# Kernel tuning notes

Hardware: AMD Instinct MI355X
Metric: run time of the kernel (lower is better)

Reference implementation:

```python
import jax, jax.numpy as jnp
import numpy as np


def setup_inputs() -> dict:
    key = jax.random.key(0)
    ks = jax.random.split(key, 8)
    B, L, I, H, O = 512, 512, 256, 1024, 1
    def glorot(k, shape, fan_sum):
        return jax.random.uniform(k, shape, jnp.float32, -1.0, 1.0) * (6.0 / fan_sum) ** 0.5
    return {
        "X": jax.random.normal(ks[0], (B, L, I), jnp.float32),
        "W_in1": glorot(ks[1], (H, I), H + I),
        "b_in1": jnp.zeros((H, 1), jnp.float32),
        "W_rec1": glorot(ks[2], (H, H), H + H),
        "W_in2": glorot(ks[3], (H, I), H + I),
        "b_in2": jnp.zeros((H, 1), jnp.float32),
        "W_rec2": glorot(ks[4], (H, H), H + H),
        "W_out": glorot(ks[5], (O, H), O + H),
        "b_out": jnp.zeros((O, 1), jnp.float32),
    }


def reference(X, W_in1, b_in1, W_rec1, W_in2, b_in2, W_rec2, W_out, b_out):
    B, L, I = X.shape
    H = W_in1.shape[0]
    Xs = jnp.swapaxes(X, 0, 1)  # (L, B, I)
    # Precompute the input-to-hidden projections for all timesteps (parallel GEMMs).
    in1 = jnp.einsum("hi,lbi->lbh", W_in1, Xs) + b_in1[:, 0]  # (L, B, H)
    in2 = jnp.einsum("hi,lbi->lbh", W_in2, Xs) + b_in2[:, 0]  # (L, B, H)
    even = (jnp.arange(L) % 2 == 0)[:, None, None]  # (L, 1, 1) broadcast mask

    def step(carry, xs):
        z12, z1, z2 = carry  # each (B, H)
        a1, a2, ev = xs
        z1n = jnp.tanh(a1 + z12 @ W_rec1.T)
        z2n = jnp.where(ev, jnp.tanh(a2 + z2 @ W_rec2.T), z2)  # branch updates only on even l
        return (z1n + z2n, z1n, z2n), None

    z0 = jnp.zeros((B, H), X.dtype)
    (z12, z1, z2), _ = jax.lax.scan(step, (z0, z0, z0), (in1, in2, even))
    z_out = jnp.tanh(z1 @ W_out.T + b_out[:, 0])  # (B, num_outputs)
    return z_out.reshape(B, 1)
```

## Files before the change

kernel.cpp:

```cpp
#include <hip/hip_runtime.h>
#include <hip/hip_bf16.h>

typedef __attribute__((ext_vector_type(8))) short bhalf8;
typedef __attribute__((ext_vector_type(4))) float fvec4;
typedef __attribute__((ext_vector_type(4))) unsigned u32x4;

static __device__ __forceinline__ unsigned short f2bf(float f) {
  unsigned u = __builtin_bit_cast(unsigned, f);
  u = (u + 0x7fffu + ((u >> 16) & 1u)) >> 16;
  return (unsigned short)u;
}
static __device__ __forceinline__ float tanh_fast(float x) {
  x = fminf(12.f, fmaxf(-12.f, x));
  float e = __expf(2.f * x);
  return (e - 1.f) / (e + 1.f);
}
static __device__ __forceinline__ fvec4 tanh4(fvec4 v) {
  fvec4 r;
  r[0] = tanh_fast(v[0]); r[1] = tanh_fast(v[1]);
  r[2] = tanh_fast(v[2]); r[3] = tanh_fast(v[3]);
  return r;
}
static __device__ __forceinline__ bhalf8 load_w8(const float* p) {
  fvec4 a = *(const fvec4*)p;
  fvec4 b = *(const fvec4*)(p + 4);
  bhalf8 r;
  r[0] = (short)f2bf(a[0]); r[1] = (short)f2bf(a[1]);
  r[2] = (short)f2bf(a[2]); r[3] = (short)f2bf(a[3]);
  r[4] = (short)f2bf(b[0]); r[5] = (short)f2bf(b[1]);
  r[6] = (short)f2bf(b[2]); r[7] = (short)f2bf(b[3]);
  return r;
}

static __device__ __forceinline__ void st_f32_coh(float* p, float v) {
  asm volatile("global_store_dword %0, %1, off sc0 sc1" :: "v"(p), "v"(v) : "memory");
}
static __device__ __forceinline__ void st_u32_coh(unsigned* p, unsigned v) {
  asm volatile("global_store_dword %0, %1, off sc0 sc1" :: "v"(p), "v"(v) : "memory");
}
static __device__ __forceinline__ void st16_coh(void* p, u32x4 v) {
  asm volatile("global_store_dwordx4 %0, %1, off sc0 sc1" :: "v"(p), "v"(v) : "memory");
}
static __device__ __forceinline__ unsigned ld_u32_coh(const unsigned* p) {
  unsigned v;
  asm volatile("global_load_dword %0, %1, off sc0 sc1\n\ts_waitcnt vmcnt(0)"
               : "=v"(v) : "v"(p) : "memory");
  return v;
}
static __device__ __forceinline__ float ld_f32_coh(const float* p) {
  float v;
  asm volatile("global_load_dword %0, %1, off sc0 sc1\n\ts_waitcnt vmcnt(0)"
               : "=v"(v) : "v"(p) : "memory");
  return v;
}
static __device__ __forceinline__ void gll16_coh(const void* g, void* lds) {
  __builtin_amdgcn_global_load_lds(
      (const __attribute__((address_space(1))) void*)g,
      (__attribute__((address_space(3))) void*)lds, 16, 0, 0x11);
}

#define MFMA16(a, b, c) __builtin_amdgcn_mfma_f32_16x16x32_bf16((a), (b), (c), 0, 0, 0)

extern "C" __global__ void __launch_bounds__(256, 1)
alarm_rnn_persist(const float* __restrict__ X, const float* __restrict__ Win1,
                  const float* __restrict__ bin1, const float* __restrict__ Wrec1,
                  const float* __restrict__ Win2, const float* __restrict__ bin2,
                  const float* __restrict__ Wrec2, const float* __restrict__ Wout,
                  const float* __restrict__ bout, float* __restrict__ out,
                  unsigned* flags, unsigned short* gbuf0, unsigned short* gbuf1,
                  unsigned short* z2b0, unsigned short* z2b1, float* z1buf)
{
  constexpr int kL = 512, kI = 256, kH = 1024;
  extern __shared__ char smem[];

  const int tid = threadIdx.x, bid = blockIdx.x;
  const int grp = bid >> 4, memb = bid & 15;
  const int lane = tid & 63, w = tid >> 6;
  const int row16 = lane & 15, kq = lane >> 4;
  const int sw = (row16 & 7) << 4;
  const int hcol = memb * 64 + w * 16 + row16;
  const int brow0 = grp * 32;

  bhalf8 w1[32], w2[32], wi1[8], wi2[8];
#pragma unroll
  for (int nt = 0; nt < 4; ++nt) {
    const size_t c = (size_t)(memb * 64 + nt * 16 + row16);
#pragma unroll
    for (int kk = 0; kk < 8; ++kk) {
      w1[nt * 8 + kk] = load_w8(Wrec1 + c * kH + w * 256 + kk * 32 + kq * 8);
      w2[nt * 8 + kk] = load_w8(Wrec2 + c * kH + w * 256 + kk * 32 + kq * 8);
    }
#pragma unroll
    for (int k2 = 0; k2 < 2; ++k2) {
      wi1[nt * 2 + k2] = load_w8(Win1 + c * kI + w * 64 + k2 * 32 + kq * 8);
      wi2[nt * 2 + k2] = load_w8(Win2 + c * kI + w * 64 + k2 * 32 + kq * 8);
    }
  }
  const float bv1 = bin1[hcol];
  const float bv2 = bin2[hcol];
  fvec4 z2c0 = {0.f, 0.f, 0.f, 0.f}, z2c1 = {0.f, 0.f, 0.f, 0.f};

  {
    int r = tid >> 3, q = tid & 7;
#pragma unroll
    for (int p = 0; p < 2; ++p) {
      const float* xp = X + (size_t)(brow0 + r) * (kL * kI) + (size_t)p * kI;
      fvec4 xv[8];
#pragma unroll
      for (int j = 0; j < 8; ++j) xv[j] = *(const fvec4*)(xp + q * 4 + j * 32);
#pragma unroll
      for (int j = 0; j < 8; ++j) {
        int i0 = q * 4 + j * 32;
        ushort4 pk;
        pk.x = f2bf(xv[j][0]); pk.y = f2bf(xv[j][1]);
        pk.z = f2bf(xv[j][2]); pk.w = f2bf(xv[j][3]);
        *(ushort4*)(smem + 131072 + p * 16384 + (r << 9) + ((i0 * 2) ^ ((r & 7) << 4))) = pk;
      }
    }
  }
  __syncthreads();

  for (int l = 0; l < kL; ++l) {
    const bool even = ((l & 1) == 0);
    const int e = l >> 1;

    {
      const unsigned short* zsrc = (l & 1) ? gbuf1 : gbuf0;
#pragma unroll
      for (int it = 0; it < 16; ++it) {
        int itx = (it + memb) & 15;
        int c = ((itx * 4 + w) << 6) + lane;
        int r = c >> 7, cbs = (c & 127) * 16;
        gll16_coh((const char*)zsrc + (((size_t)(brow0 + r)) << 11) + (cbs ^ ((r & 7) << 4)),
                  smem + ((itx * 4 + w) << 10));
      }
      if (even) {
        const unsigned short* z2src = (e & 1) ? z2b1 : z2b0;
#pragma unroll
        for (int it = 0; it < 16; ++it) {
          int itx = (it + memb) & 15;
          int c = ((itx * 4 + w) << 6) + lane;
          int r = c >> 7, cbs = (c & 127) * 16;
          gll16_coh((const char*)z2src + (((size_t)(brow0 + r)) << 11) + (cbs ^ ((r & 7) << 4)),
                    smem + 65536 + ((itx * 4 + w) << 10));
        }
      }
      __builtin_amdgcn_sched_barrier(0);
    }

    const char* xb = smem + 131072 + ((l & 1) << 14);
    fvec4 acc[8], c2a[8];
#pragma unroll
    for (int t = 0; t < 8; ++t) { acc[t] = {0.f, 0.f, 0.f, 0.f}; c2a[t] = {0.f, 0.f, 0.f, 0.f}; }
#pragma unroll
    for (int k2 = 0; k2 < 2; ++k2) {
      int cbx = (w * 2 + k2) * 64 + kq * 16;
      bhalf8 xa0 = *(const bhalf8*)(xb + (row16 << 9) + (cbx ^ sw));
      bhalf8 xa1 = *(const bhalf8*)(xb + ((16 + row16) << 9) + (cbx ^ sw));
#pragma unroll
      for (int nt = 0; nt < 4; ++nt) {
        acc[nt * 2] = MFMA16(xa0, wi1[nt * 2 + k2], acc[nt * 2]);
        acc[nt * 2 + 1] = MFMA16(xa1, wi1[nt * 2 + k2], acc[nt * 2 + 1]);
      }
      if (even) {
#pragma unroll
        for (int nt = 0; nt < 4; ++nt) {
          c2a[nt * 2] = MFMA16(xa0, wi2[nt * 2 + k2], c2a[nt * 2]);
          c2a[nt * 2 + 1] = MFMA16(xa1, wi2[nt * 2 + k2], c2a[nt * 2 + 1]);
        }
      }
    }
    asm volatile("s_waitcnt vmcnt(0)" ::: "memory");
    __builtin_amdgcn_sched_barrier(0);
    __syncthreads();

#pragma unroll
    for (int kk = 0; kk < 8; ++kk) {
      int cb = (w * 8 + kk) * 64 + kq * 16;
      bhalf8 a0 = *(const bhalf8*)(smem + (row16 << 11) + (cb ^ sw));
      bhalf8 a1 = *(const bhalf8*)(smem + ((16 + row16) << 11) + (cb ^ sw));
#pragma unroll
      for (int nt = 0; nt < 4; ++nt) {
        acc[nt * 2] = MFMA16(a0, w1[nt * 8 + kk], acc[nt * 2]);
        acc[nt * 2 + 1] = MFMA16(a1, w1[nt * 8 + kk], acc[nt * 2 + 1]);
      }
    }
    if (even) {
#pragma unroll
      for (int kk = 0; kk < 8; ++kk) {
        int cb = (w * 8 + kk) * 64 + kq * 16;
        bhalf8 a0 = *(const bhalf8*)(smem + 65536 + (row16 << 11) + (cb ^ sw));
        bhalf8 a1 = *(const bhalf8*)(smem + 65536 + ((16 + row16) << 11) + (cb ^ sw));
#pragma unroll
        for (int nt = 0; nt < 4; ++nt) {
          c2a[nt * 2] = MFMA16(a0, w2[nt * 8 + kk], c2a[nt * 2]);
          c2a[nt * 2 + 1] = MFMA16(a1, w2[nt * 8 + kk], c2a[nt * 2 + 1]);
        }
      }
    }

    __syncthreads();
#pragma unroll
    for (int nt = 0; nt < 4; ++nt)
#pragma unroll
      for (int mt = 0; mt < 2; ++mt) {
        int base = (((nt * 2 + mt) * 4 + w) << 10);
        fvec4 v = acc[nt * 2 + mt];
#pragma unroll
        for (int i = 0; i < 4; ++i)
          *(float*)(smem + base + (((kq * 4 + i) * 16 + row16) << 2)) = v[i];
        if (even) {
          fvec4 v2 = c2a[nt * 2 + mt];
#pragma unroll
          for (int i = 0; i < 4; ++i)
            *(float*)(smem + 32768 + base + (((kq * 4 + i) * 16 + row16) << 2)) = v2[i];
        }
      }
    __syncthreads();

    fvec4 s0 = {0.f, 0.f, 0.f, 0.f}, s1 = s0;
#pragma unroll
    for (int ws = 0; ws < 4; ++ws) {
      int b0 = (((w * 2 + 0) * 4 + ws) << 10), b1 = (((w * 2 + 1) * 4 + ws) << 10);
#pragma unroll
      for (int i = 0; i < 4; ++i) {
        s0[i] += *(const float*)(smem + b0 + (((kq * 4 + i) * 16 + row16) << 2));
        s1[i] += *(const float*)(smem + b1 + (((kq * 4 + i) * 16 + row16) << 2));
      }
    }
#pragma unroll
    for (int i = 0; i < 4; ++i) { s0[i] += bv1; s1[i] += bv1; }
    fvec4 z1n0 = tanh4(s0), z1n1 = tanh4(s1);
    if (even) {
      fvec4 t0 = {0.f, 0.f, 0.f, 0.f}, t1 = t0;
#pragma unroll
      for (int ws = 0; ws < 4; ++ws) {
        int b0 = 32768 + (((w * 2 + 0) * 4 + ws) << 10), b1 = 32768 + (((w * 2 + 1) * 4 + ws) << 10);
#pragma unroll
        for (int i = 0; i < 4; ++i) {
          t0[i] += *(const float*)(smem + b0 + (((kq * 4 + i) * 16 + row16) << 2));
          t1[i] += *(const float*)(smem + b1 + (((kq * 4 + i) * 16 + row16) << 2));
        }
      }
#pragma unroll
      for (int i = 0; i < 4; ++i) { t0[i] += bv2; t1[i] += bv2; }
      z2c0 = tanh4(t0);
      z2c1 = tanh4(t1);
    }

    if (l < kL - 1) {
      const int colb = (w * 16 + row16) * 2;
#pragma unroll
      for (int i = 0; i < 4; ++i) {
        int r0 = kq * 4 + i, r1 = 16 + kq * 4 + i;
        *(unsigned short*)(smem + 65536 + r0 * 128 + (colb ^ ((r0 & 7) << 4))) = f2bf(z1n0[i] + z2c0[i]);
        *(unsigned short*)(smem + 65536 + r1 * 128 + (colb ^ ((r1 & 7) << 4))) = f2bf(z1n1[i] + z2c1[i]);
      }
      if (even) {
#pragma unroll
        for (int i = 0; i < 4; ++i) {
          int r0 = kq * 4 + i, r1 = 16 + kq * 4 + i;
          *(unsigned short*)(smem + 69632 + r0 * 128 + (colb ^ ((r0 & 7) << 4))) = f2bf(z2c0[i]);
          *(unsigned short*)(smem + 69632 + r1 * 128 + (colb ^ ((r1 & 7) << 4))) = f2bf(z2c1[i]);
        }
      }
      __syncthreads();
      {
        int r = tid >> 3, s = tid & 7;
        u32x4 v = *(const u32x4*)(smem + 65536 + r * 128 + ((s * 16) ^ ((r & 7) << 4)));
        unsigned short* dst = (l & 1) ? gbuf0 : gbuf1;
        st16_coh((char*)dst + (((size_t)(brow0 + r)) << 11) + memb * 128 + s * 16, v);
        if (even) {
          u32x4 v2 = *(const u32x4*)(smem + 69632 + r * 128 + ((s * 16) ^ ((r & 7) << 4)));
          unsigned short* z2dst = (e & 1) ? z2b0 : z2b1;
          st16_coh((char*)z2dst + (((size_t)(brow0 + r)) << 11) + memb * 128 + s * 16, v2);
        }
      }
    } else {
#pragma unroll
      for (int i = 0; i < 4; ++i) {
        st_f32_coh(z1buf + (size_t)(brow0 + kq * 4 + i) * kH + hcol, z1n0[i]);
        st_f32_coh(z1buf + (size_t)(brow0 + 16 + kq * 4 + i) * kH + hcol, z1n1[i]);
      }
    }
    asm volatile("s_waitcnt vmcnt(0)" ::: "memory");
    __syncthreads();
    if (tid == 0) st_u32_coh(flags + grp * 16 + memb, (unsigned)(l + 1));

    if (l + 2 < kL) {
      const int xr = tid >> 3, xq = tid & 7;
      const float* xp = X + (size_t)(brow0 + xr) * (kL * kI) + (size_t)(l + 2) * kI;
      fvec4 xv[8];
#pragma unroll
      for (int j = 0; j < 8; ++j) xv[j] = *(const fvec4*)(xp + xq * 4 + j * 32);
#pragma unroll
      for (int j = 0; j < 8; ++j) {
        int i0 = xq * 4 + j * 32;
        ushort4 pk;
        pk.x = f2bf(xv[j][0]); pk.y = f2bf(xv[j][1]);
        pk.z = f2bf(xv[j][2]); pk.w = f2bf(xv[j][3]);
        *(ushort4*)(smem + 131072 + ((l & 1) << 14) + (xr << 9) + ((i0 * 2) ^ ((xr & 7) << 4))) = pk;
      }
    }

    {
      const unsigned tgt = (unsigned)(l + 1);
      const unsigned* fp = flags + grp * 16 + (lane & 15);
      for (;;) {
        unsigned v = (lane < 16) ? ld_u32_coh(fp) : tgt;
        bool ok = (lane >= 16) || ((lane & 15) == memb) || (v >= tgt);
        if (__all(ok)) break;
        __builtin_amdgcn_s_sleep(1);
      }
      __builtin_amdgcn_sched_barrier(0);
    }
  }

  if (memb == 0) {
    int r = tid >> 3, q = tid & 7;
    const float* zr = z1buf + (size_t)(brow0 + r) * kH;
    float s = 0.f;
    for (int h = q * 128; h < q * 128 + 128; ++h) s += ld_f32_coh(zr + h) * Wout[h];
    s += __shfl_xor(s, 1);
    s += __shfl_xor(s, 2);
    s += __shfl_xor(s, 4);
    if (q == 0) out[brow0 + r] = tanh_fast(s + bout[0]);
  }
}

extern "C" void kernel_launch(void* const* d_in, const int* in_sizes, int n_in,
                              void* d_out, int out_size, void* d_ws, size_t ws_size,
                              hipStream_t stream) {
  const float* X = (const float*)d_in[0];
  const float* Win1 = (const float*)d_in[1];
  const float* bin1 = (const float*)d_in[2];
  const float* Wrec1 = (const float*)d_in[3];
  const float* Win2 = (const float*)d_in[4];
  const float* bin2 = (const float*)d_in[5];
  const float* Wrec2 = (const float*)d_in[6];
  const float* Wout = (const float*)d_in[7];
  const float* bout = (const float*)d_in[8];
  float* out = (float*)d_out;

  char* ws = (char*)d_ws;
  unsigned* flags = (unsigned*)ws;
  unsigned short* gbuf0 = (unsigned short*)(ws + 4096);
  unsigned short* gbuf1 = (unsigned short*)(ws + 4096 + (1 << 20));
  unsigned short* z2b0 = (unsigned short*)(ws + 4096 + (2 << 20));
  unsigned short* z2b1 = (unsigned short*)(ws + 4096 + (3 << 20));
  float* z1buf = (float*)(ws + 4096 + (4 << 20));

  (void)hipMemsetAsync(flags, 0, 4096, stream);
  (void)hipMemsetAsync(gbuf0, 0, (size_t)512 * 1024 * 2, stream);
  (void)hipMemsetAsync(z2b0, 0, (size_t)512 * 1024 * 2, stream);

  (void)hipFuncSetAttribute((const void*)alarm_rnn_persist,
                            hipFuncAttributeMaxDynamicSharedMemorySize, 163840);

  alarm_rnn_persist<<<dim3(256), dim3(256), 163840, stream>>>(
      X, Win1, bin1, Wrec1, Win2, bin2, Wrec2, Wout, bout, out,
      flags, gbuf0, gbuf1, z2b0, z2b1, z1buf);
}
```

Baseline: 5.173 ms.

## Double threads per block to 512 and split the K reduction across 8 waves

Each persistent block now runs 8 waves instead of 4. The hidden-dimension reduction is split 8 ways, so each wave holds half as many register-resident weight fragments and issues half as many MFMAs per step. The cross-wave partial-sum reduction, the tanh epilogue and the global stores are reworked so that waves split work by row half and column tile, and the z1 and z2 stores are spread across thread halves. This aims to cut per-step latency on the serial recurrence. In exchange it adds a larger LDS reduction and an extra barrier per step.

```diff
diff --git a/kernel.cpp b/kernel.cpp
--- a/kernel.cpp
+++ b/kernel.cpp
@@ -61,7 +61,7 @@
 
 #define MFMA16(a, b, c) __builtin_amdgcn_mfma_f32_16x16x32_bf16((a), (b), (c), 0, 0, 0)
 
-extern "C" __global__ void __launch_bounds__(256, 1)
+extern "C" __global__ void __launch_bounds__(512, 1)
 alarm_rnn_persist(const float* __restrict__ X, const float* __restrict__ Win1,
                   const float* __restrict__ bin1, const float* __restrict__ Wrec1,
                   const float* __restrict__ Win2, const float* __restrict__ bin2,
@@ -78,42 +78,37 @@
   const int lane = tid & 63, w = tid >> 6;
   const int row16 = lane & 15, kq = lane >> 4;
   const int sw = (row16 & 7) << 4;
-  const int hcol = memb * 64 + w * 16 + row16;
+  const int ntw = w >> 1, mtw = w & 1;
+  const int hcolf = memb * 64 + ntw * 16 + row16;
   const int brow0 = grp * 32;
 
-  bhalf8 w1[32], w2[32], wi1[8], wi2[8];
+  bhalf8 w1[16], w2[16], wi1[4], wi2[4];
 #pragma unroll
   for (int nt = 0; nt < 4; ++nt) {
     const size_t c = (size_t)(memb * 64 + nt * 16 + row16);
 #pragma unroll
-    for (int kk = 0; kk < 8; ++kk) {
-      w1[nt * 8 + kk] = load_w8(Wrec1 + c * kH + w * 256 + kk * 32 + kq * 8);
-      w2[nt * 8 + kk] = load_w8(Wrec2 + c * kH + w * 256 + kk * 32 + kq * 8);
-    }
-#pragma unroll
-    for (int k2 = 0; k2 < 2; ++k2) {
-      wi1[nt * 2 + k2] = load_w8(Win1 + c * kI + w * 64 + k2 * 32 + kq * 8);
-      wi2[nt * 2 + k2] = load_w8(Win2 + c * kI + w * 64 + k2 * 32 + kq * 8);
-    }
+    for (int kk = 0; kk < 4; ++kk) {
+      w1[nt * 4 + kk] = load_w8(Wrec1 + c * kH + w * 128 + kk * 32 + kq * 8);
+      w2[nt * 4 + kk] = load_w8(Wrec2 + c * kH + w * 128 + kk * 32 + kq * 8);
+    }
+    wi1[nt] = load_w8(Win1 + c * kI + w * 32 + kq * 8);
+    wi2[nt] = load_w8(Win2 + c * kI + w * 32 + kq * 8);
   }
-  const float bv1 = bin1[hcol];
-  const float bv2 = bin2[hcol];
-  fvec4 z2c0 = {0.f, 0.f, 0.f, 0.f}, z2c1 = {0.f, 0.f, 0.f, 0.f};
+  const float bv1 = bin1[hcolf];
+  const float bv2 = bin2[hcolf];
+  fvec4 z2c = {0.f, 0.f, 0.f, 0.f};
 
   {
-    int r = tid >> 3, q = tid & 7;
+    int r = tid >> 4, t = tid & 15;
 #pragma unroll
     for (int p = 0; p < 2; ++p) {
       const float* xp = X + (size_t)(brow0 + r) * (kL * kI) + (size_t)p * kI;
-      fvec4 xv[8];
-#pragma unroll
-      for (int j = 0; j < 8; ++j) xv[j] = *(const fvec4*)(xp + q * 4 + j * 32);
-#pragma unroll
-      for (int j = 0; j < 8; ++j) {
-        int i0 = q * 4 + j * 32;
+#pragma unroll
+      for (int j = 0; j < 4; ++j) {
+        fvec4 v = *(const fvec4*)(xp + t * 4 + j * 64);
         ushort4 pk;
-        pk.x = f2bf(xv[j][0]); pk.y = f2bf(xv[j][1]);
-        pk.z = f2bf(xv[j][2]); pk.w = f2bf(xv[j][3]);
+        pk.x = f2bf(v[0]); pk.y = f2bf(v[1]); pk.z = f2bf(v[2]); pk.w = f2bf(v[3]);
+        int i0 = t * 4 + j * 64;
         *(ushort4*)(smem + 131072 + p * 16384 + (r << 9) + ((i0 * 2) ^ ((r & 7) << 4))) = pk;
       }
     }
@@ -127,22 +122,22 @@
     {
       const unsigned short* zsrc = (l & 1) ? gbuf1 : gbuf0;
 #pragma unroll
-      for (int it = 0; it < 16; ++it) {
-        int itx = (it + memb) & 15;
-        int c = ((itx * 4 + w) << 6) + lane;
+      for (int it = 0; it < 8; ++it) {
+        int ci = ((it + memb) & 7) * 8 + w;
+        int c = (ci << 6) + lane;
         int r = c >> 7, cbs = (c & 127) * 16;
         gll16_coh((const char*)zsrc + (((size_t)(brow0 + r)) << 11) + (cbs ^ ((r & 7) << 4)),
-                  smem + ((itx * 4 + w) << 10));
+                  smem + ci * 1024 + lane * 16);
       }
       if (even) {
         const unsigned short* z2src = (e & 1) ? z2b1 : z2b0;
 #pragma unroll
-        for (int it = 0; it < 16; ++it) {
-          int itx = (it + memb) & 15;
-          int c = ((itx * 4 + w) << 6) + lane;
+        for (int it = 0; it < 8; ++it) {
+          int ci = ((it + memb) & 7) * 8 + w;
+          int c = (ci << 6) + lane;
           int r = c >> 7, cbs = (c & 127) * 16;
           gll16_coh((const char*)z2src + (((size_t)(brow0 + r)) << 11) + (cbs ^ ((r & 7) << 4)),
-                    smem + 65536 + ((itx * 4 + w) << 10));
+                    smem + 65536 + ci * 1024 + lane * 16);
         }
       }
       __builtin_amdgcn_sched_barrier(0);
@@ -152,21 +147,20 @@
     fvec4 acc[8], c2a[8];
 #pragma unroll
     for (int t = 0; t < 8; ++t) { acc[t] = {0.f, 0.f, 0.f, 0.f}; c2a[t] = {0.f, 0.f, 0.f, 0.f}; }
-#pragma unroll
-    for (int k2 = 0; k2 < 2; ++k2) {
-      int cbx = (w * 2 + k2) * 64 + kq * 16;
+    {
+      int cbx = w * 64 + kq * 16;
       bhalf8 xa0 = *(const bhalf8*)(xb + (row16 << 9) + (cbx ^ sw));
       bhalf8 xa1 = *(const bhalf8*)(xb + ((16 + row16) << 9) + (cbx ^ sw));
 #pragma unroll
       for (int nt = 0; nt < 4; ++nt) {
-        acc[nt * 2] = MFMA16(xa0, wi1[nt * 2 + k2], acc[nt * 2]);
-        acc[nt * 2 + 1] = MFMA16(xa1, wi1[nt * 2 + k2], acc[nt * 2 + 1]);
+        acc[nt * 2] = MFMA16(xa0, wi1[nt], acc[nt * 2]);
+        acc[nt * 2 + 1] = MFMA16(xa1, wi1[nt], acc[nt * 2 + 1]);
       }
       if (even) {
 #pragma unroll
         for (int nt = 0; nt < 4; ++nt) {
-          c2a[nt * 2] = MFMA16(xa0, wi2[nt * 2 + k2], c2a[nt * 2]);
-          c2a[nt * 2 + 1] = MFMA16(xa1, wi2[nt * 2 + k2], c2a[nt * 2 + 1]);
+          c2a[nt * 2] = MFMA16(xa0, wi2[nt], c2a[nt * 2]);
+          c2a[nt * 2 + 1] = MFMA16(xa1, wi2[nt], c2a[nt * 2 + 1]);
         }
       }
     }
@@ -175,131 +169,113 @@
     __syncthreads();
 
 #pragma unroll
-    for (int kk = 0; kk < 8; ++kk) {
-      int cb = (w * 8 + kk) * 64 + kq * 16;
+    for (int kk = 0; kk < 4; ++kk) {
+      int cb = (w * 4 + kk) * 64 + kq * 16;
       bhalf8 a0 = *(const bhalf8*)(smem + (row16 << 11) + (cb ^ sw));
       bhalf8 a1 = *(const bhalf8*)(smem + ((16 + row16) << 11) + (cb ^ sw));
 #pragma unroll
       for (int nt = 0; nt < 4; ++nt) {
-        acc[nt * 2] = MFMA16(a0, w1[nt * 8 + kk], acc[nt * 2]);
-        acc[nt * 2 + 1] = MFMA16(a1, w1[nt * 8 + kk], acc[nt * 2 + 1]);
+        acc[nt * 2] = MFMA16(a0, w1[nt * 4 + kk], acc[nt * 2]);
+        acc[nt * 2 + 1] = MFMA16(a1, w1[nt * 4 + kk], acc[nt * 2 + 1]);
       }
     }
     if (even) {
 #pragma unroll
-      for (int kk = 0; kk < 8; ++kk) {
-        int cb = (w * 8 + kk) * 64 + kq * 16;
+      for (int kk = 0; kk < 4; ++kk) {
+        int cb = (w * 4 + kk) * 64 + kq * 16;
         bhalf8 a0 = *(const bhalf8*)(smem + 65536 + (row16 << 11) + (cb ^ sw));
         bhalf8 a1 = *(const bhalf8*)(smem + 65536 + ((16 + row16) << 11) + (cb ^ sw));
 #pragma unroll
         for (int nt = 0; nt < 4; ++nt) {
-          c2a[nt * 2] = MFMA16(a0, w2[nt * 8 + kk], c2a[nt * 2]);
-          c2a[nt * 2 + 1] = MFMA16(a1, w2[nt * 8 + kk], c2a[nt * 2 + 1]);
+          c2a[nt * 2] = MFMA16(a0, w2[nt * 4 + kk], c2a[nt * 2]);
+          c2a[nt * 2 + 1] = MFMA16(a1, w2[nt * 4 + kk], c2a[nt * 2 + 1]);
         }
       }
     }
 
     __syncthreads();
 #pragma unroll
-    for (int nt = 0; nt < 4; ++nt)
-#pragma unroll
-      for (int mt = 0; mt < 2; ++mt) {
-        int base = (((nt * 2 + mt) * 4 + w) << 10);
-        fvec4 v = acc[nt * 2 + mt];
+    for (int t8 = 0; t8 < 8; ++t8) {
+      int base = (t8 * 8 + w) << 10;
+      fvec4 v = acc[t8];
+#pragma unroll
+      for (int i = 0; i < 4; ++i)
+        *(float*)(smem + base + (((kq * 4 + i) * 16 + row16) << 2)) = v[i];
+      if (even) {
+        fvec4 v2 = c2a[t8];
 #pragma unroll
         for (int i = 0; i < 4; ++i)
-          *(float*)(smem + base + (((kq * 4 + i) * 16 + row16) << 2)) = v[i];
-        if (even) {
-          fvec4 v2 = c2a[nt * 2 + mt];
-#pragma unroll
-          for (int i = 0; i < 4; ++i)
-            *(float*)(smem + 32768 + base + (((kq * 4 + i) * 16 + row16) << 2)) = v2[i];
-        }
-      }
-    __syncthreads();
-
-    fvec4 s0 = {0.f, 0.f, 0.f, 0.f}, s1 = s0;
-#pragma unroll
-    for (int ws = 0; ws < 4; ++ws) {
-      int b0 = (((w * 2 + 0) * 4 + ws) << 10), b1 = (((w * 2 + 1) * 4 + ws) << 10);
+          *(float*)(smem + 65536 + base + (((kq * 4 + i) * 16 + row16) << 2)) = v2[i];
+      }
+    }
+    __syncthreads();
+
+    fvec4 s0 = {0.f, 0.f, 0.f, 0.f};
+#pragma unroll
+    for (int ws = 0; ws < 8; ++ws) {
+      int b = (w * 8 + ws) << 10;
+#pragma unroll
+      for (int i = 0; i < 4; ++i)
+        s0[i] += *(const float*)(smem + b + (((kq * 4 + i) * 16 + row16) << 2));
+    }
+#pragma unroll
+    for (int i = 0; i < 4; ++i) s0[i] += bv1;
+    fvec4 z1n = tanh4(s0);
+    if (even) {
+      fvec4 t0 = {0.f, 0.f, 0.f, 0.f};
+#pragma unroll
+      for (int ws = 0; ws < 8; ++ws) {
+        int b = 65536 + ((w * 8 + ws) << 10);
+#pragma unroll
+        for (int i = 0; i < 4; ++i)
+          t0[i] += *(const float*)(smem + b + (((kq * 4 + i) * 16 + row16) << 2));
+      }
+#pragma unroll
+      for (int i = 0; i < 4; ++i) t0[i] += bv2;
+      z2c = tanh4(t0);
+    }
+    __syncthreads();
+
+    if (l < kL - 1) {
+      const int cb2 = (ntw * 16 + row16) * 2;
 #pragma unroll
       for (int i = 0; i < 4; ++i) {
-        s0[i] += *(const float*)(smem + b0 + (((kq * 4 + i) * 16 + row16) << 2));
-        s1[i] += *(const float*)(smem + b1 + (((kq * 4 + i) * 16 + row16) << 2));
-      }
-    }
-#pragma unroll
-    for (int i = 0; i < 4; ++i) { s0[i] += bv1; s1[i] += bv1; }
-    fvec4 z1n0 = tanh4(s0), z1n1 = tanh4(s1);
-    if (even) {
-      fvec4 t0 = {0.f, 0.f, 0.f, 0.f}, t1 = t0;
-#pragma unroll
-      for (int ws = 0; ws < 4; ++ws) {
-        int b0 = 32768 + (((w * 2 + 0) * 4 + ws) << 10), b1 = 32768 + (((w * 2 + 1) * 4 + ws) << 10);
-#pragma unroll
-        for (int i = 0; i < 4; ++i) {
-          t0[i] += *(const float*)(smem + b0 + (((kq * 4 + i) * 16 + row16) << 2));
-          t1[i] += *(const float*)(smem + b1 + (((kq * 4 + i) * 16 + row16) << 2));
-        }
-      }
-#pragma unroll
-      for (int i = 0; i < 4; ++i) { t0[i] += bv2; t1[i] += bv2; }
-      z2c0 = tanh4(t0);
-      z2c1 = tanh4(t1);
-    }
-
-    if (l < kL - 1) {
-      const int colb = (w * 16 + row16) * 2;
-#pragma unroll
-      for (int i = 0; i < 4; ++i) {
-        int r0 = kq * 4 + i, r1 = 16 + kq * 4 + i;
-        *(unsigned short*)(smem + 65536 + r0 * 128 + (colb ^ ((r0 & 7) << 4))) = f2bf(z1n0[i] + z2c0[i]);
-        *(unsigned short*)(smem + 65536 + r1 * 128 + (colb ^ ((r1 & 7) << 4))) = f2bf(z1n1[i] + z2c1[i]);
-      }
-      if (even) {
-#pragma unroll
-        for (int i = 0; i < 4; ++i) {
-          int r0 = kq * 4 + i, r1 = 16 + kq * 4 + i;
-          *(unsigned short*)(smem + 69632 + r0 * 128 + (colb ^ ((r0 & 7) << 4))) = f2bf(z2c0[i]);
-          *(unsigned short*)(smem + 69632 + r1 * 128 + (colb ^ ((r1 & 7) << 4))) = f2bf(z2c1[i]);
-        }
+        int r0 = mtw * 16 + kq * 4 + i;
+        *(unsigned short*)(smem + r0 * 128 + (cb2 ^ ((r0 & 7) << 4))) = f2bf(z1n[i] + z2c[i]);
+        if (even)
+          *(unsigned short*)(smem + 4096 + r0 * 128 + (cb2 ^ ((r0 & 7) << 4))) = f2bf(z2c[i]);
       }
       __syncthreads();
-      {
-        int r = tid >> 3, s = tid & 7;
-        u32x4 v = *(const u32x4*)(smem + 65536 + r * 128 + ((s * 16) ^ ((r & 7) << 4)));
+      if (tid < 256) {
+        int r = tid >> 3, s8 = tid & 7;
+        u32x4 v = *(const u32x4*)(smem + r * 128 + ((s8 * 16) ^ ((r & 7) << 4)));
         unsigned short* dst = (l & 1) ? gbuf0 : gbuf1;
-        st16_coh((char*)dst + (((size_t)(brow0 + r)) << 11) + memb * 128 + s * 16, v);
-        if (even) {
-          u32x4 v2 = *(const u32x4*)(smem + 69632 + r * 128 + ((s * 16) ^ ((r & 7) << 4)));
-          unsigned short* z2dst = (e & 1) ? z2b0 : z2b1;
-          st16_coh((char*)z2dst + (((size_t)(brow0 + r)) << 11) + memb * 128 + s * 16, v2);
-        }
+        st16_coh((char*)dst + (((size_t)(brow0 + r)) << 11) + memb * 128 + s8 * 16, v);
+      } else if (even) {
+        int t2 = tid - 256, r = t2 >> 3, s8 = t2 & 7;
+        u32x4 v2 = *(const u32x4*)(smem + 4096 + r * 128 + ((s8 * 16) ^ ((r & 7) << 4)));
+        unsigned short* z2dst = (e & 1) ? z2b0 : z2b1;
+        st16_coh((char*)z2dst + (((size_t)(brow0 + r)) << 11) + memb * 128 + s8 * 16, v2);
       }
     } else {
 #pragma unroll
-      for (int i = 0; i < 4; ++i) {
-        st_f32_coh(z1buf + (size_t)(brow0 + kq * 4 + i) * kH + hcol, z1n0[i]);
-        st_f32_coh(z1buf + (size_t)(brow0 + 16 + kq * 4 + i) * kH + hcol, z1n1[i]);
-      }
+      for (int i = 0; i < 4; ++i)
+        st_f32_coh(z1buf + (size_t)(brow0 + mtw * 16 + kq * 4 + i) * kH + hcolf, z1n[i]);
     }
     asm volatile("s_waitcnt vmcnt(0)" ::: "memory");
     __syncthreads();
     if (tid == 0) st_u32_coh(flags + grp * 16 + memb, (unsigned)(l + 1));
 
     if (l + 2 < kL) {
-      const int xr = tid >> 3, xq = tid & 7;
-      const float* xp = X + (size_t)(brow0 + xr) * (kL * kI) + (size_t)(l + 2) * kI;
-      fvec4 xv[8];
-#pragma unroll
-      for (int j = 0; j < 8; ++j) xv[j] = *(const fvec4*)(xp + xq * 4 + j * 32);
-#pragma unroll
-      for (int j = 0; j < 8; ++j) {
-        int i0 = xq * 4 + j * 32;
+      int r = tid >> 4, t = tid & 15;
+      const float* xp = X + (size_t)(brow0 + r) * (kL * kI) + (size_t)(l + 2) * kI;
+#pragma unroll
+      for (int j = 0; j < 4; ++j) {
+        fvec4 v = *(const fvec4*)(xp + t * 4 + j * 64);
         ushort4 pk;
-        pk.x = f2bf(xv[j][0]); pk.y = f2bf(xv[j][1]);
-        pk.z = f2bf(xv[j][2]); pk.w = f2bf(xv[j][3]);
-        *(ushort4*)(smem + 131072 + ((l & 1) << 14) + (xr << 9) + ((i0 * 2) ^ ((xr & 7) << 4))) = pk;
+        pk.x = f2bf(v[0]); pk.y = f2bf(v[1]); pk.z = f2bf(v[2]); pk.w = f2bf(v[3]);
+        int i0 = t * 4 + j * 64;
+        *(ushort4*)(smem + 131072 + ((l & 1) << 14) + (r << 9) + ((i0 * 2) ^ ((r & 7) << 4))) = pk;
       }
     }
 
@@ -317,13 +293,14 @@
   }
 
   if (memb == 0) {
-    int r = tid >> 3, q = tid & 7;
+    int r = tid >> 4, q = tid & 15;
     const float* zr = z1buf + (size_t)(brow0 + r) * kH;
     float s = 0.f;
-    for (int h = q * 128; h < q * 128 + 128; ++h) s += ld_f32_coh(zr + h) * Wout[h];
+    for (int h = q * 64; h < q * 64 + 64; ++h) s += ld_f32_coh(zr + h) * Wout[h];
     s += __shfl_xor(s, 1);
     s += __shfl_xor(s, 2);
     s += __shfl_xor(s, 4);
+    s += __shfl_xor(s, 8);
     if (q == 0) out[brow0 + r] = tanh_fast(s + bout[0]);
   }
 }
@@ -357,7 +334,7 @@
   (void)hipFuncSetAttribute((const void*)alarm_rnn_persist,
                             hipFuncAttributeMaxDynamicSharedMemorySize, 163840);
 
-  alarm_rnn_persist<<<dim3(256), dim3(256), 163840, stream>>>(
+  alarm_rnn_persist<<<dim3(256), dim3(512), 163840, stream>>>(
       X, Win1, bin1, Wrec1, Win2, bin2, Wrec2, Wout, bout, out,
       flags, gbuf0, gbuf1, z2b0, z2b1, z1buf);
 }
```

New measurement: 8.256 ms. +59.6%, slower.
